# Kernel tuning notes

Hardware: AMD Instinct MI355X
Metric: run time of the kernel (lower is better)

The kernel has to match this reference:

```python
import jax, jax.numpy as jnp
import numpy as np

N_NODES = 100000


def _graph_conv(x, W, b, src, dst, norm):
    # DGL GraphConv(norm='left'): scale source features by 1/out_degree,
    # aggregate (sum over incoming edges). in_feats > out_feats so weight
    # multiply happens before aggregation (mathematically equivalent either way).
    h = x @ W  # [N, out]
    msg = (h * norm[:, None])[src]  # gather per-edge messages [E, out]
    agg = jax.ops.segment_sum(msg, dst, num_segments=N_NODES)
    return agg + b


def setup_inputs() -> dict:
    key = jax.random.key(0)
    ks = jax.random.split(key, 10)
    in_f, hid_f, out_f = 256, 128, 64
    n_edges = 1_600_000
    feat = jax.random.normal(ks[0], (N_NODES, in_f), dtype=jnp.float32)
    src = jax.random.randint(ks[1], (n_edges,), 0, N_NODES, dtype=jnp.int32)
    dst = jax.random.randint(ks[2], (n_edges,), 0, N_NODES, dtype=jnp.int32)
    noise = jax.random.normal(ks[3], (N_NODES, out_f), dtype=jnp.float32)
    s1 = 1.0 / np.sqrt(in_f)
    s2 = 1.0 / np.sqrt(hid_f)
    W_shared = jax.random.uniform(ks[4], (in_f, hid_f), minval=-s1, maxval=s1, dtype=jnp.float32)
    b_shared = jnp.zeros((hid_f,), jnp.float32)
    W_mu = jax.random.uniform(ks[5], (hid_f, out_f), minval=-s2, maxval=s2, dtype=jnp.float32)
    b_mu = jnp.zeros((out_f,), jnp.float32)
    W_ls = jax.random.uniform(ks[6], (hid_f, out_f), minval=-s2, maxval=s2, dtype=jnp.float32)
    b_ls = jnp.zeros((out_f,), jnp.float32)
    return {"feat": feat, "W_shared": W_shared, "b_shared": b_shared,
            "W_mu": W_mu, "b_mu": b_mu, "W_ls": W_ls, "b_ls": b_ls,
            "noise": noise, "src": src, "dst": dst}


def reference(feat, W_shared, b_shared, W_mu, b_mu, W_ls, b_ls, noise, src, dst):
    # left-norm: 1 / out_degree (clamped to >= 1, as DGL does)
    deg_out = jax.ops.segment_sum(jnp.ones_like(src, jnp.float32), src,
                                  num_segments=N_NODES)
    norm = 1.0 / jnp.maximum(deg_out, 1.0)
    # shared first GraphConv with ReLU activation
    h = jax.nn.relu(_graph_conv(feat, W_shared, b_shared, src, dst, norm))
    # two heads (no activation)
    mu = _graph_conv(h, W_mu, b_mu, src, dst, norm)
    log_sigma = _graph_conv(h, W_ls, b_ls, src, dst, norm)
    # reparameterized sample
    return mu + noise * jnp.exp(log_sigma)
```

## Files before the change

### kernel.cpp

```cpp
#include <hip/hip_runtime.h>
#include <hip/hip_bf16.h>
#include <math.h>

typedef __attribute__((ext_vector_type(8))) short short8;
typedef __attribute__((ext_vector_type(4))) float f32x4;

__device__ __forceinline__ unsigned short f2bf(float f) {
    unsigned int u = __float_as_uint(f);
    u += 0x7FFF + ((u >> 16) & 1);
    return (unsigned short)(u >> 16);
}
__device__ __forceinline__ float b2f(unsigned short s) {
    return __uint_as_float(((unsigned int)s) << 16);
}
__device__ __forceinline__ unsigned int f2bf2(float a, float b) {
    __hip_bfloat162 h = __float22bfloat162_rn(make_float2(a, b));
    return *(unsigned int*)&h;
}
__device__ __forceinline__ void gl_lds16(const void* g, void* l) {
    __builtin_amdgcn_global_load_lds(
        (const __attribute__((address_space(1))) void*)g,
        (__attribute__((address_space(3))) void*)l, 16, 0, 0);
}

#define EB 8192
#define BSH 10
#define NBKT 128

__global__ __launch_bounds__(256)
void k1_hist(const int* __restrict__ src, const int* __restrict__ dst,
             int* __restrict__ bhist, int* __restrict__ degS, int E) {
    __shared__ int hist[NBKT];
    int t = threadIdx.x;
    if (t < NBKT) hist[t] = 0;
    __syncthreads();
    int base = blockIdx.x * EB;
    int end = min(base + EB, E);
    for (int e = base + 4 * t; e < end; e += 1024) {
        if (e + 3 < end) {
            int4 d4 = *(const int4*)&dst[e];
            int4 s4 = *(const int4*)&src[e];
            atomicAdd(&hist[d4.x >> BSH], 1);
            atomicAdd(&hist[d4.y >> BSH], 1);
            atomicAdd(&hist[d4.z >> BSH], 1);
            atomicAdd(&hist[d4.w >> BSH], 1);
            atomicAdd(&degS[s4.x], 1);
            atomicAdd(&degS[s4.y], 1);
            atomicAdd(&degS[s4.z], 1);
            atomicAdd(&degS[s4.w], 1);
        } else {
            for (int q = e; q < end; ++q) {
                atomicAdd(&hist[dst[q] >> BSH], 1);
                atomicAdd(&degS[src[q]], 1);
            }
        }
    }
    __syncthreads();
    if (t < NBKT) bhist[(size_t)blockIdx.x * NBKT + t] = hist[t];
}

__global__ __launch_bounds__(128)
void kc1_totals(const int* __restrict__ bhist, int* __restrict__ totals, int PB) {
    int t = threadIdx.x;
    int slice = (PB + 7) / 8;
    int b0 = blockIdx.x * slice;
    int b1 = min(b0 + slice, PB);
    int s = 0;
    for (int blk = b0; blk < b1; ++blk) s += bhist[(size_t)blk * NBKT + t];
    if (s) atomicAdd(&totals[t], s);
}

__global__ __launch_bounds__(128)
void kc2_scan(const int* __restrict__ totals, int* __restrict__ bbase_d) {
    __shared__ int s[128];
    int t = threadIdx.x;
    int v = totals[t];
    s[t] = v;
    __syncthreads();
    for (int off = 1; off < 128; off <<= 1) {
        int u = (t >= off) ? s[t - off] : 0;
        __syncthreads();
        s[t] += u;
        __syncthreads();
    }
    bbase_d[t] = s[t] - v;
}

__global__ __launch_bounds__(256)
void kc3_boff(const int* __restrict__ bhist, const int* __restrict__ bbase_d,
              int* __restrict__ boffT, int PB) {
    __shared__ int sums[256];
    int b = blockIdx.x;
    int t = threadIdx.x;
    int v = (t < PB) ? bhist[(size_t)t * NBKT + b] : 0;
    sums[t] = v;
    __syncthreads();
    for (int off = 1; off < 256; off <<= 1) {
        int u = (t >= off) ? sums[t - off] : 0;
        __syncthreads();
        sums[t] += u;
        __syncthreads();
    }
    if (t < PB) boffT[(size_t)b * PB + t] = bbase_d[b] + sums[t] - v;
}

__global__ __launch_bounds__(256)
void k_norm(const int* __restrict__ degS, float* __restrict__ norm, int N) {
    int i = blockIdx.x * 256 + threadIdx.x;
    if (i < N) {
        int d = degS[i];
        norm[i] = 1.0f / (float)(d > 1 ? d : 1);
    }
}

__global__ __launch_bounds__(256)
void k2_scatter(const int* __restrict__ src, const int* __restrict__ dst,
                const int* __restrict__ boffT, int* __restrict__ parr,
                int E, int PB) {
    __shared__ int cnt[NBKT];
    int t = threadIdx.x;
    int blk = blockIdx.x;
    if (t < NBKT) cnt[t] = boffT[(size_t)t * PB + blk];
    __syncthreads();
    int base = blk * EB;
    int end = min(base + EB, E);
    for (int e = base + 4 * t; e < end; e += 1024) {
        if (e + 3 < end) {
            int4 s4 = *(const int4*)&src[e];
            int4 d4 = *(const int4*)&dst[e];
            int p0 = atomicAdd(&cnt[d4.x >> BSH], 1);
            parr[p0] = (s4.x << BSH) | (d4.x & (1024 - 1));
            int p1 = atomicAdd(&cnt[d4.y >> BSH], 1);
            parr[p1] = (s4.y << BSH) | (d4.y & (1024 - 1));
            int p2 = atomicAdd(&cnt[d4.z >> BSH], 1);
            parr[p2] = (s4.z << BSH) | (d4.z & (1024 - 1));
            int p3 = atomicAdd(&cnt[d4.w >> BSH], 1);
            parr[p3] = (s4.w << BSH) | (d4.w & (1024 - 1));
        } else {
            for (int q = e; q < end; ++q) {
                int sv = src[q], dv = dst[q];
                int pd = atomicAdd(&cnt[dv >> BSH], 1);
                parr[pd] = (sv << BSH) | (dv & (1024 - 1));
            }
        }
    }
}

__global__ __launch_bounds__(1024)
void k3_dst(const int* __restrict__ parr, const int* __restrict__ totals,
            const int* __restrict__ bbase_d, int* __restrict__ row_off,
            int* __restrict__ col, int N, int E) {
    __shared__ int hist[1024], sc[1024];
    int b = blockIdx.x, t = threadIdx.x;
    if (b == 0 && t == 0) row_off[N] = E;
    int ne = totals[b];
    int ebase = bbase_d[b];
    hist[t] = 0;
    __syncthreads();
    for (int i = t; i < ne; i += 1024)
        atomicAdd(&hist[parr[ebase + i] & 1023], 1);
    __syncthreads();
    int h = hist[t];
    sc[t] = h;
    __syncthreads();
    for (int off = 1; off < 1024; off <<= 1) {
        int u = (t >= off) ? sc[t - off] : 0;
        __syncthreads();
        sc[t] += u;
        __syncthreads();
    }
    int excl = sc[t] - h;
    int node = b * 1024 + t;
    if (node < N) row_off[node] = ebase + excl;
    hist[t] = ebase + excl;
    __syncthreads();
    for (int i = t; i < ne; i += 1024) {
        int pr = parr[ebase + i];
        int slot = atomicAdd(&hist[pr & 1023], 1);
        col[slot] = pr >> BSH;
    }
}


__global__ __launch_bounds__(256)
void k_wprep(const float* __restrict__ Wsh, const float* __restrict__ Wmu,
             const float* __restrict__ Wls, unsigned short* __restrict__ W1T,
             unsigned short* __restrict__ W2T) {
    int b = blockIdx.x, t = threadIdx.x;
    if (b < 128) {
        W1T[(size_t)b * 256 + t] = f2bf(Wsh[(size_t)t * 128 + b]);
    } else {
        int n = b - 128;
        if (t < 128) {
            float v = (n < 64) ? Wmu[(size_t)t * 64 + n]
                               : Wls[(size_t)t * 64 + (n - 64)];
            W2T[(size_t)n * 128 + t] = f2bf(v);
        }
    }
}

__global__ __launch_bounds__(256)
void k_gemm1(const float* __restrict__ A, int M,
             const unsigned short* __restrict__ W1T,
             const float* __restrict__ norm, unsigned short* __restrict__ outb) {
    __shared__ char ldsA[64 * 1040];
    const int w = threadIdx.x >> 6;
    const int lane = threadIdx.x & 63;
    const int quad = lane >> 4;
    const int l16 = lane & 15;
    const int cl = w * 16 + l16;
    const int r0 = blockIdx.x * 64;

#pragma unroll
    for (int i = 0; i < 16; ++i) {
        int row = r0 + w * 16 + i;
        if (row >= M) row = M - 1;
        const char* g = (const char*)A + (size_t)row * 1024 + lane * 16;
        char* l = ldsA + (w * 16 + i) * 1040 + lane * 16;
        gl_lds16(g, l);
    }

    short8 bw[2][8];
#pragma unroll
    for (int hf = 0; hf < 2; ++hf) {
        const unsigned short* wp = W1T + (size_t)(hf * 64 + cl) * 256 + quad * 8;
#pragma unroll
        for (int ks = 0; ks < 8; ++ks)
            bw[hf][ks] = *(const short8*)(wp + ks * 32);
    }
    __syncthreads();

    f32x4 acc[4][2];
#pragma unroll
    for (int m = 0; m < 4; ++m) {
        acc[m][0] = (f32x4){0.f, 0.f, 0.f, 0.f};
        acc[m][1] = (f32x4){0.f, 0.f, 0.f, 0.f};
    }
#pragma unroll
    for (int ks = 0; ks < 8; ++ks) {
#pragma unroll
        for (int m = 0; m < 4; ++m) {
            const float* pr = (const float*)(ldsA + (m * 16 + l16) * 1040 +
                                             (ks * 32 + quad * 8) * 4);
            float4 x = *(const float4*)pr;
            float4 y = *(const float4*)(pr + 4);
            union { short8 v; unsigned int u[4]; } c;
            c.u[0] = f2bf2(x.x, x.y);
            c.u[1] = f2bf2(x.z, x.w);
            c.u[2] = f2bf2(y.x, y.y);
            c.u[3] = f2bf2(y.z, y.w);
            acc[m][0] = __builtin_amdgcn_mfma_f32_16x16x32_bf16(bw[0][ks], c.v, acc[m][0], 0, 0, 0);
            acc[m][1] = __builtin_amdgcn_mfma_f32_16x16x32_bf16(bw[1][ks], c.v, acc[m][1], 0, 0, 0);
        }
    }
    const int colbase = w * 16 + quad * 4;
#pragma unroll
    for (int m = 0; m < 4; ++m) {
        int row = r0 + m * 16 + l16;
        if (row < M) {
            float nm = norm[row];
            ushort4 o0, o1;
            o0.x = f2bf(acc[m][0][0] * nm); o0.y = f2bf(acc[m][0][1] * nm);
            o0.z = f2bf(acc[m][0][2] * nm); o0.w = f2bf(acc[m][0][3] * nm);
            o1.x = f2bf(acc[m][1][0] * nm); o1.y = f2bf(acc[m][1][1] * nm);
            o1.z = f2bf(acc[m][1][2] * nm); o1.w = f2bf(acc[m][1][3] * nm);
            *(ushort4*)&outb[(size_t)row * 128 + colbase] = o0;
            *(ushort4*)&outb[(size_t)row * 128 + 64 + colbase] = o1;
        }
    }
}

__global__ __launch_bounds__(256)
void k_gemm2(const unsigned short* __restrict__ A, int M,
             const unsigned short* __restrict__ W2T,
             const float* __restrict__ norm, unsigned short* __restrict__ outb) {
    __shared__ char ldsB[16 * 1040];
    const int w = threadIdx.x >> 6;
    const int lane = threadIdx.x & 63;
    const int quad = lane >> 4;
    const int l16 = lane & 15;
    const int cl = w * 16 + l16;
    const int r0 = blockIdx.x * 64;

#pragma unroll
    for (int i = 0; i < 4; ++i) {
        int c = w * 4 + i;
        int crow = r0 + c * 4;
        if (crow + 4 > M) crow = M - 4;
        const char* g = (const char*)A + (size_t)crow * 256 + lane * 16;
        char* l = ldsB + c * 1040 + lane * 16;
        gl_lds16(g, l);
    }

    short8 bw[2][4];
#pragma unroll
    for (int hf = 0; hf < 2; ++hf) {
        const unsigned short* wp = W2T + (size_t)(hf * 64 + cl) * 128 + quad * 8;
#pragma unroll
        for (int ks = 0; ks < 4; ++ks)
            bw[hf][ks] = *(const short8*)(wp + ks * 32);
    }
    __syncthreads();

    f32x4 acc[4][2];
#pragma unroll
    for (int m = 0; m < 4; ++m) {
        acc[m][0] = (f32x4){0.f, 0.f, 0.f, 0.f};
        acc[m][1] = (f32x4){0.f, 0.f, 0.f, 0.f};
    }
#pragma unroll
    for (int ks = 0; ks < 4; ++ks) {
#pragma unroll
        for (int m = 0; m < 4; ++m) {
            int row = m * 16 + l16;
            short8 af = *(const short8*)(ldsB + (row >> 2) * 1040 + (row & 3) * 256 +
                                         (ks * 32 + quad * 8) * 2);
            acc[m][0] = __builtin_amdgcn_mfma_f32_16x16x32_bf16(bw[0][ks], af, acc[m][0], 0, 0, 0);
            acc[m][1] = __builtin_amdgcn_mfma_f32_16x16x32_bf16(bw[1][ks], af, acc[m][1], 0, 0, 0);
        }
    }
    const int colbase = w * 16 + quad * 4;
#pragma unroll
    for (int m = 0; m < 4; ++m) {
        int row = r0 + m * 16 + l16;
        if (row < M) {
            float nm = norm[row];
            ushort4 o0, o1;
            o0.x = f2bf(acc[m][0][0] * nm); o0.y = f2bf(acc[m][0][1] * nm);
            o0.z = f2bf(acc[m][0][2] * nm); o0.w = f2bf(acc[m][0][3] * nm);
            o1.x = f2bf(acc[m][1][0] * nm); o1.y = f2bf(acc[m][1][1] * nm);
            o1.z = f2bf(acc[m][1][2] * nm); o1.w = f2bf(acc[m][1][3] * nm);
            *(ushort4*)&outb[(size_t)row * 128 + colbase] = o0;
            *(ushort4*)&outb[(size_t)row * 128 + 64 + colbase] = o1;
        }
    }
}

__global__ __launch_bounds__(256)
void k_spmm_relu(const int* __restrict__ row_off, const int* __restrict__ col,
                 const unsigned short* __restrict__ hxb, const float* __restrict__ bias,
                 unsigned short* __restrict__ hb, int N) {
    int g = (blockIdx.x * blockDim.x + threadIdx.x) >> 5;
    int l = threadIdx.x & 31;
    if (g >= N) return;
    int e0 = row_off[g], e1 = row_off[g + 1];
    const ushort4* base = (const ushort4*)hxb;
    float4 acc = make_float4(0.f, 0.f, 0.f, 0.f);
    int e = e0;
    for (; e + 7 < e1; e += 8) {
        ushort4 v0 = base[(size_t)col[e] * 32 + l];
        ushort4 v1 = base[(size_t)col[e + 1] * 32 + l];
        ushort4 v2 = base[(size_t)col[e + 2] * 32 + l];
        ushort4 v3 = base[(size_t)col[e + 3] * 32 + l];
        ushort4 v4 = base[(size_t)col[e + 4] * 32 + l];
        ushort4 v5 = base[(size_t)col[e + 5] * 32 + l];
        ushort4 v6 = base[(size_t)col[e + 6] * 32 + l];
        ushort4 v7 = base[(size_t)col[e + 7] * 32 + l];
        acc.x += ((b2f(v0.x) + b2f(v1.x)) + (b2f(v2.x) + b2f(v3.x))) +
                 ((b2f(v4.x) + b2f(v5.x)) + (b2f(v6.x) + b2f(v7.x)));
        acc.y += ((b2f(v0.y) + b2f(v1.y)) + (b2f(v2.y) + b2f(v3.y))) +
                 ((b2f(v4.y) + b2f(v5.y)) + (b2f(v6.y) + b2f(v7.y)));
        acc.z += ((b2f(v0.z) + b2f(v1.z)) + (b2f(v2.z) + b2f(v3.z))) +
                 ((b2f(v4.z) + b2f(v5.z)) + (b2f(v6.z) + b2f(v7.z)));
        acc.w += ((b2f(v0.w) + b2f(v1.w)) + (b2f(v2.w) + b2f(v3.w))) +
                 ((b2f(v4.w) + b2f(v5.w)) + (b2f(v6.w) + b2f(v7.w)));
    }
    for (; e + 1 < e1; e += 2) {
        ushort4 a = base[(size_t)col[e] * 32 + l];
        ushort4 b = base[(size_t)col[e + 1] * 32 + l];
        acc.x += b2f(a.x) + b2f(b.x);
        acc.y += b2f(a.y) + b2f(b.y);
        acc.z += b2f(a.z) + b2f(b.z);
        acc.w += b2f(a.w) + b2f(b.w);
    }
    if (e < e1) {
        ushort4 a = base[(size_t)col[e] * 32 + l];
        acc.x += b2f(a.x); acc.y += b2f(a.y); acc.z += b2f(a.z); acc.w += b2f(a.w);
    }
    float4 bi = ((const float4*)bias)[l];
    ushort4 r;
    r.x = f2bf(fmaxf(acc.x + bi.x, 0.f));
    r.y = f2bf(fmaxf(acc.y + bi.y, 0.f));
    r.z = f2bf(fmaxf(acc.z + bi.z, 0.f));
    r.w = f2bf(fmaxf(acc.w + bi.w, 0.f));
    ((ushort4*)hb)[(size_t)g * 32 + l] = r;
}

__global__ __launch_bounds__(256)
void k_spmm_out(const int* __restrict__ row_off, const int* __restrict__ col,
                const unsigned short* __restrict__ hcb, const float* __restrict__ bmu,
                const float* __restrict__ bls, const float* __restrict__ noise,
                float* __restrict__ out, int N) {
    int g = (blockIdx.x * blockDim.x + threadIdx.x) >> 5;
    int l = threadIdx.x & 31;
    if (g >= N) return;
    int e0 = row_off[g], e1 = row_off[g + 1];
    const ushort4* base = (const ushort4*)hcb;
    float4 acc = make_float4(0.f, 0.f, 0.f, 0.f);
    int e = e0;
    for (; e + 7 < e1; e += 8) {
        ushort4 v0 = base[(size_t)col[e] * 32 + l];
        ushort4 v1 = base[(size_t)col[e + 1] * 32 + l];
        ushort4 v2 = base[(size_t)col[e + 2] * 32 + l];
        ushort4 v3 = base[(size_t)col[e + 3] * 32 + l];
        ushort4 v4 = base[(size_t)col[e + 4] * 32 + l];
        ushort4 v5 = base[(size_t)col[e + 5] * 32 + l];
        ushort4 v6 = base[(size_t)col[e + 6] * 32 + l];
        ushort4 v7 = base[(size_t)col[e + 7] * 32 + l];
        acc.x += ((b2f(v0.x) + b2f(v1.x)) + (b2f(v2.x) + b2f(v3.x))) +
                 ((b2f(v4.x) + b2f(v5.x)) + (b2f(v6.x) + b2f(v7.x)));
        acc.y += ((b2f(v0.y) + b2f(v1.y)) + (b2f(v2.y) + b2f(v3.y))) +
                 ((b2f(v4.y) + b2f(v5.y)) + (b2f(v6.y) + b2f(v7.y)));
        acc.z += ((b2f(v0.z) + b2f(v1.z)) + (b2f(v2.z) + b2f(v3.z))) +
                 ((b2f(v4.z) + b2f(v5.z)) + (b2f(v6.z) + b2f(v7.z)));
        acc.w += ((b2f(v0.w) + b2f(v1.w)) + (b2f(v2.w) + b2f(v3.w))) +
                 ((b2f(v4.w) + b2f(v5.w)) + (b2f(v6.w) + b2f(v7.w)));
    }
    for (; e + 1 < e1; e += 2) {
        ushort4 a = base[(size_t)col[e] * 32 + l];
        ushort4 b = base[(size_t)col[e + 1] * 32 + l];
        acc.x += b2f(a.x) + b2f(b.x);
        acc.y += b2f(a.y) + b2f(b.y);
        acc.z += b2f(a.z) + b2f(b.z);
        acc.w += b2f(a.w) + b2f(b.w);
    }
    if (e < e1) {
        ushort4 a = base[(size_t)col[e] * 32 + l];
        acc.x += b2f(a.x); acc.y += b2f(a.y); acc.z += b2f(a.z); acc.w += b2f(a.w);
    }
    int lane64 = threadIdx.x & 63;
    int p = (lane64 + 16) & 63;
    float lx = __shfl(acc.x, p, 64);
    float ly = __shfl(acc.y, p, 64);
    float lz = __shfl(acc.z, p, 64);
    float lw = __shfl(acc.w, p, 64);
    if (l < 16) {
        float4 bm = ((const float4*)bmu)[l];
        float4 bl = ((const float4*)bls)[l];
        float4 nz = ((const float4*)noise)[(size_t)g * 16 + l];
        float4 o;
        o.x = (acc.x + bm.x) + nz.x * expf(lx + bl.x);
        o.y = (acc.y + bm.y) + nz.y * expf(ly + bl.y);
        o.z = (acc.z + bm.z) + nz.z * expf(lz + bl.z);
        o.w = (acc.w + bm.w) + nz.w * expf(lw + bl.w);
        ((float4*)out)[(size_t)g * 16 + l] = o;
    }
}

static inline char* align64(char* p) {
    return (char*)(((uintptr_t)p + 63) & ~(uintptr_t)63);
}

extern "C" void kernel_launch(void* const* d_in, const int* in_sizes, int n_in,
                              void* d_out, int out_size, void* d_ws, size_t ws_size,
                              hipStream_t stream) {
    const float* feat  = (const float*)d_in[0];
    const float* Wsh   = (const float*)d_in[1];
    const float* bsh   = (const float*)d_in[2];
    const float* Wmu   = (const float*)d_in[3];
    const float* bmu   = (const float*)d_in[4];
    const float* Wls   = (const float*)d_in[5];
    const float* bls   = (const float*)d_in[6];
    const float* noise = (const float*)d_in[7];
    const int*   src   = (const int*)d_in[8];
    const int*   dst   = (const int*)d_in[9];
    float* out = (float*)d_out;

    const int N = in_sizes[0] / 256;
    const int E = in_sizes[8];
    const int PB = (E + EB - 1) / EB;

    char* p = (char*)d_ws;
    float* norm   = (float*)p;                  p += (size_t)N * 4;         p = align64(p);
    int* row_off  = (int*)p;                    p += (size_t)(N + 4) * 4;   p = align64(p);
    int* degS     = (int*)p;                    p += (size_t)N * 4;
    int* totals   = (int*)p;                    p += 128 * 4;
    int* bbase_d  = (int*)p;                    p += 128 * 4;               p = align64(p);
    unsigned short* W1T = (unsigned short*)p;   p += (size_t)128 * 256 * 2;
    unsigned short* W2T = (unsigned short*)p;   p += (size_t)128 * 128 * 2;
    p = align64(p);
    int* bhist    = (int*)p;                    p += (size_t)PB * NBKT * 4; p = align64(p);
    int* boffT    = (int*)p;                    p += (size_t)NBKT * PB * 4; p = align64(p);
    int* parr     = (int*)p;                    p += (size_t)E * 4;
    int* col      = (int*)p;                    p += (size_t)E * 4;         p = align64(p);
    unsigned short* hxb = (unsigned short*)p;
    unsigned short* hb  = (unsigned short*)d_out;

    hipMemsetAsync(degS, 0, (size_t)N * 4 + 128 * 4, stream);
    k_wprep<<<256, 256, 0, stream>>>(Wsh, Wmu, Wls, W1T, W2T);
    k1_hist<<<PB, 256, 0, stream>>>(src, dst, bhist, degS, E);
    kc1_totals<<<8, 128, 0, stream>>>(bhist, totals, PB);
    kc2_scan<<<1, 128, 0, stream>>>(totals, bbase_d);
    kc3_boff<<<NBKT, 256, 0, stream>>>(bhist, bbase_d, boffT, PB);
    k_norm<<<(N + 255) / 256, 256, 0, stream>>>(degS, norm, N);
    k2_scatter<<<PB, 256, 0, stream>>>(src, dst, boffT, parr, E, PB);
    k3_dst<<<NBKT, 1024, 0, stream>>>(parr, totals, bbase_d, row_off, col, N, E);

    int gtiles = (N + 63) / 64;
    k_gemm1<<<gtiles, 256, 0, stream>>>(feat, N, W1T, norm, hxb);
    k_spmm_relu<<<(N * 32 + 255) / 256, 256, 0, stream>>>(row_off, col, hxb, bsh, hb, N);
    k_gemm2<<<gtiles, 256, 0, stream>>>(hb, N, W2T, norm, hxb);
    k_spmm_out<<<(N * 32 + 255) / 256, 256, 0, stream>>>(row_off, col, hxb, bmu, bls, noise, out, N);
}
```

Baseline: 486.9 us.

## Compute out-degree via bucketed sort instead of global atomics; shrink buckets

Replaces the per-edge global atomicAdd on the out-degree array with a second bucketed counting pass over source ids: source bucket histograms sit next to the destination ones, edges are scattered into a 16-bit local-id array, and a new per-bucket kernel counts degrees in LDS and writes norm. It also shrinks buckets to 512 nodes and edge blocks to 2048 edges, which means more blocks and 1024-thread scans. The goal is to avoid contended random global atomics and the memset of the degree array, at the cost of extra scatter writes and an extra kernel launch.

Result: faster. 444.6 us (-8.7%).

```diff
diff --git a/kernel.cpp b/kernel.cpp
--- a/kernel.cpp
+++ b/kernel.cpp
@@ -23,16 +23,17 @@
         (__attribute__((address_space(3))) void*)l, 16, 0, 0);
 }
 
-#define EB 8192
-#define BSH 10
-#define NBKT 128
+#define EB 2048
+#define SH 9
+#define BSZ 512
 
 __global__ __launch_bounds__(256)
 void k1_hist(const int* __restrict__ src, const int* __restrict__ dst,
-             int* __restrict__ bhist, int* __restrict__ degS, int E) {
-    __shared__ int hist[NBKT];
+             int* __restrict__ bhist, int E, int NB2) {
+    __shared__ int hist[512];
     int t = threadIdx.x;
-    if (t < NBKT) hist[t] = 0;
+    int NB = NB2 >> 1;
+    for (int i = t; i < NB2; i += 256) hist[i] = 0;
     __syncthreads();
     int base = blockIdx.x * EB;
     int end = min(base + EB, E);
@@ -40,87 +41,84 @@
         if (e + 3 < end) {
             int4 d4 = *(const int4*)&dst[e];
             int4 s4 = *(const int4*)&src[e];
-            atomicAdd(&hist[d4.x >> BSH], 1);
-            atomicAdd(&hist[d4.y >> BSH], 1);
-            atomicAdd(&hist[d4.z >> BSH], 1);
-            atomicAdd(&hist[d4.w >> BSH], 1);
-            atomicAdd(&degS[s4.x], 1);
-            atomicAdd(&degS[s4.y], 1);
-            atomicAdd(&degS[s4.z], 1);
-            atomicAdd(&degS[s4.w], 1);
+            atomicAdd(&hist[d4.x >> SH], 1);
+            atomicAdd(&hist[d4.y >> SH], 1);
+            atomicAdd(&hist[d4.z >> SH], 1);
+            atomicAdd(&hist[d4.w >> SH], 1);
+            atomicAdd(&hist[NB + (s4.x >> SH)], 1);
+            atomicAdd(&hist[NB + (s4.y >> SH)], 1);
+            atomicAdd(&hist[NB + (s4.z >> SH)], 1);
+            atomicAdd(&hist[NB + (s4.w >> SH)], 1);
         } else {
             for (int q = e; q < end; ++q) {
-                atomicAdd(&hist[dst[q] >> BSH], 1);
-                atomicAdd(&degS[src[q]], 1);
+                atomicAdd(&hist[dst[q] >> SH], 1);
+                atomicAdd(&hist[NB + (src[q] >> SH)], 1);
             }
         }
     }
     __syncthreads();
-    if (t < NBKT) bhist[(size_t)blockIdx.x * NBKT + t] = hist[t];
-}
-
-__global__ __launch_bounds__(128)
-void kc1_totals(const int* __restrict__ bhist, int* __restrict__ totals, int PB) {
+    for (int i = t; i < NB2; i += 256)
+        bhist[(size_t)blockIdx.x * NB2 + i] = hist[i];
+}
+
+__global__ __launch_bounds__(512)
+void kc1_totals(const int* __restrict__ bhist, int* __restrict__ totals,
+                int PB, int NB2) {
     int t = threadIdx.x;
-    int slice = (PB + 7) / 8;
+    if (t >= NB2) return;
+    int slice = (PB + 15) / 16;
     int b0 = blockIdx.x * slice;
     int b1 = min(b0 + slice, PB);
     int s = 0;
-    for (int blk = b0; blk < b1; ++blk) s += bhist[(size_t)blk * NBKT + t];
+    for (int blk = b0; blk < b1; ++blk) s += bhist[(size_t)blk * NB2 + t];
     if (s) atomicAdd(&totals[t], s);
 }
 
-__global__ __launch_bounds__(128)
-void kc2_scan(const int* __restrict__ totals, int* __restrict__ bbase_d) {
-    __shared__ int s[128];
+__global__ __launch_bounds__(512)
+void kc2_scan(const int* __restrict__ totals, int* __restrict__ bbase, int NB) {
+    __shared__ int s[512];
     int t = threadIdx.x;
-    int v = totals[t];
+    int half = t >> 8;
+    int idx = t & 255;
+    int v = (idx < NB) ? totals[half * NB + idx] : 0;
     s[t] = v;
     __syncthreads();
-    for (int off = 1; off < 128; off <<= 1) {
-        int u = (t >= off) ? s[t - off] : 0;
+    for (int off = 1; off < 256; off <<= 1) {
+        int u = (idx >= off) ? s[t - off] : 0;
         __syncthreads();
         s[t] += u;
         __syncthreads();
     }
-    bbase_d[t] = s[t] - v;
-}
-
-__global__ __launch_bounds__(256)
-void kc3_boff(const int* __restrict__ bhist, const int* __restrict__ bbase_d,
-              int* __restrict__ boffT, int PB) {
-    __shared__ int sums[256];
+    if (idx < NB) bbase[half * NB + idx] = s[t] - v;
+}
+
+__global__ __launch_bounds__(1024)
+void kc3_boff(const int* __restrict__ bhist, const int* __restrict__ bbase,
+              int* __restrict__ boffT, int PB, int NB2) {
+    __shared__ int sums[1024];
     int b = blockIdx.x;
     int t = threadIdx.x;
-    int v = (t < PB) ? bhist[(size_t)t * NBKT + b] : 0;
+    int v = (t < PB) ? bhist[(size_t)t * NB2 + b] : 0;
     sums[t] = v;
     __syncthreads();
-    for (int off = 1; off < 256; off <<= 1) {
+    for (int off = 1; off < 1024; off <<= 1) {
         int u = (t >= off) ? sums[t - off] : 0;
         __syncthreads();
         sums[t] += u;
         __syncthreads();
     }
-    if (t < PB) boffT[(size_t)b * PB + t] = bbase_d[b] + sums[t] - v;
-}
-
-__global__ __launch_bounds__(256)
-void k_norm(const int* __restrict__ degS, float* __restrict__ norm, int N) {
-    int i = blockIdx.x * 256 + threadIdx.x;
-    if (i < N) {
-        int d = degS[i];
-        norm[i] = 1.0f / (float)(d > 1 ? d : 1);
-    }
+    if (t < PB) boffT[(size_t)b * PB + t] = bbase[b] + sums[t] - v;
 }
 
 __global__ __launch_bounds__(256)
 void k2_scatter(const int* __restrict__ src, const int* __restrict__ dst,
                 const int* __restrict__ boffT, int* __restrict__ parr,
-                int E, int PB) {
-    __shared__ int cnt[NBKT];
+                unsigned short* __restrict__ sarr, int E, int PB, int NB2) {
+    __shared__ int cnt[512];
     int t = threadIdx.x;
     int blk = blockIdx.x;
-    if (t < NBKT) cnt[t] = boffT[(size_t)t * PB + blk];
+    int NB = NB2 >> 1;
+    for (int i = t; i < NB2; i += 256) cnt[i] = boffT[(size_t)i * PB + blk];
     __syncthreads();
     int base = blk * EB;
     int end = min(base + EB, E);
@@ -128,19 +126,29 @@
         if (e + 3 < end) {
             int4 s4 = *(const int4*)&src[e];
             int4 d4 = *(const int4*)&dst[e];
-            int p0 = atomicAdd(&cnt[d4.x >> BSH], 1);
-            parr[p0] = (s4.x << BSH) | (d4.x & (1024 - 1));
-            int p1 = atomicAdd(&cnt[d4.y >> BSH], 1);
-            parr[p1] = (s4.y << BSH) | (d4.y & (1024 - 1));
-            int p2 = atomicAdd(&cnt[d4.z >> BSH], 1);
-            parr[p2] = (s4.z << BSH) | (d4.z & (1024 - 1));
-            int p3 = atomicAdd(&cnt[d4.w >> BSH], 1);
-            parr[p3] = (s4.w << BSH) | (d4.w & (1024 - 1));
+            int p0 = atomicAdd(&cnt[d4.x >> SH], 1);
+            parr[p0] = (s4.x << SH) | (d4.x & (BSZ - 1));
+            int p1 = atomicAdd(&cnt[d4.y >> SH], 1);
+            parr[p1] = (s4.y << SH) | (d4.y & (BSZ - 1));
+            int p2 = atomicAdd(&cnt[d4.z >> SH], 1);
+            parr[p2] = (s4.z << SH) | (d4.z & (BSZ - 1));
+            int p3 = atomicAdd(&cnt[d4.w >> SH], 1);
+            parr[p3] = (s4.w << SH) | (d4.w & (BSZ - 1));
+            int q0 = atomicAdd(&cnt[NB + (s4.x >> SH)], 1);
+            sarr[q0] = (unsigned short)(s4.x & (BSZ - 1));
+            int q1 = atomicAdd(&cnt[NB + (s4.y >> SH)], 1);
+            sarr[q1] = (unsigned short)(s4.y & (BSZ - 1));
+            int q2 = atomicAdd(&cnt[NB + (s4.z >> SH)], 1);
+            sarr[q2] = (unsigned short)(s4.z & (BSZ - 1));
+            int q3 = atomicAdd(&cnt[NB + (s4.w >> SH)], 1);
+            sarr[q3] = (unsigned short)(s4.w & (BSZ - 1));
         } else {
             for (int q = e; q < end; ++q) {
                 int sv = src[q], dv = dst[q];
-                int pd = atomicAdd(&cnt[dv >> BSH], 1);
-                parr[pd] = (sv << BSH) | (dv & (1024 - 1));
+                int pd = atomicAdd(&cnt[dv >> SH], 1);
+                parr[pd] = (sv << SH) | (dv & (BSZ - 1));
+                int ps = atomicAdd(&cnt[NB + (sv >> SH)], 1);
+                sarr[ps] = (unsigned short)(sv & (BSZ - 1));
             }
         }
     }
@@ -148,36 +156,57 @@
 
 __global__ __launch_bounds__(1024)
 void k3_dst(const int* __restrict__ parr, const int* __restrict__ totals,
-            const int* __restrict__ bbase_d, int* __restrict__ row_off,
+            const int* __restrict__ bbase, int* __restrict__ row_off,
             int* __restrict__ col, int N, int E) {
-    __shared__ int hist[1024], sc[1024];
+    __shared__ int hist[512], sc[512];
     int b = blockIdx.x, t = threadIdx.x;
     if (b == 0 && t == 0) row_off[N] = E;
     int ne = totals[b];
-    int ebase = bbase_d[b];
-    hist[t] = 0;
+    int ebase = bbase[b];
+    if (t < 512) hist[t] = 0;
     __syncthreads();
     for (int i = t; i < ne; i += 1024)
-        atomicAdd(&hist[parr[ebase + i] & 1023], 1);
-    __syncthreads();
-    int h = hist[t];
-    sc[t] = h;
-    __syncthreads();
-    for (int off = 1; off < 1024; off <<= 1) {
-        int u = (t >= off) ? sc[t - off] : 0;
+        atomicAdd(&hist[parr[ebase + i] & (BSZ - 1)], 1);
+    __syncthreads();
+    int h = 0;
+    if (t < 512) { h = hist[t]; sc[t] = h; }
+    __syncthreads();
+    for (int off = 1; off < 512; off <<= 1) {
+        int u = (t < 512 && t >= off) ? sc[t - off] : 0;
         __syncthreads();
-        sc[t] += u;
+        if (t < 512) sc[t] += u;
         __syncthreads();
     }
-    int excl = sc[t] - h;
-    int node = b * 1024 + t;
-    if (node < N) row_off[node] = ebase + excl;
-    hist[t] = ebase + excl;
+    if (t < 512) {
+        int excl = sc[t] - h;
+        int node = b * BSZ + t;
+        if (node < N) row_off[node] = ebase + excl;
+        hist[t] = ebase + excl;
+    }
     __syncthreads();
     for (int i = t; i < ne; i += 1024) {
         int pr = parr[ebase + i];
-        int slot = atomicAdd(&hist[pr & 1023], 1);
-        col[slot] = pr >> BSH;
+        int slot = atomicAdd(&hist[pr & (BSZ - 1)], 1);
+        col[slot] = pr >> SH;
+    }
+}
+
+__global__ __launch_bounds__(1024)
+void k3_src(const unsigned short* __restrict__ sarr, const int* __restrict__ totals_s,
+            const int* __restrict__ bbase_s, float* __restrict__ norm, int N) {
+    __shared__ int hist[512];
+    int b = blockIdx.x, t = threadIdx.x;
+    int ne = totals_s[b];
+    int sb = bbase_s[b];
+    if (t < 512) hist[t] = 0;
+    __syncthreads();
+    for (int i = t; i < ne; i += 1024)
+        atomicAdd(&hist[sarr[sb + i]], 1);
+    __syncthreads();
+    int node = b * BSZ + t;
+    if (t < 512 && node < N) {
+        int d = hist[t];
+        norm[node] = 1.0f / (float)(d > 1 ? d : 1);
     }
 }
 
@@ -469,32 +498,34 @@
     const int N = in_sizes[0] / 256;
     const int E = in_sizes[8];
     const int PB = (E + EB - 1) / EB;
+    const int NB = (N + BSZ - 1) / BSZ;
+    const int NB2 = 2 * NB;
 
     char* p = (char*)d_ws;
-    float* norm   = (float*)p;                  p += (size_t)N * 4;         p = align64(p);
-    int* row_off  = (int*)p;                    p += (size_t)(N + 4) * 4;   p = align64(p);
-    int* degS     = (int*)p;                    p += (size_t)N * 4;
-    int* totals   = (int*)p;                    p += 128 * 4;
-    int* bbase_d  = (int*)p;                    p += 128 * 4;               p = align64(p);
+    float* norm   = (float*)p;                  p += (size_t)N * 4;          p = align64(p);
+    int* row_off  = (int*)p;                    p += (size_t)(N + 4) * 4;    p = align64(p);
+    int* totals   = (int*)p;                    p += 512 * 4;
+    int* bbase    = (int*)p;                    p += 512 * 4;                p = align64(p);
     unsigned short* W1T = (unsigned short*)p;   p += (size_t)128 * 256 * 2;
     unsigned short* W2T = (unsigned short*)p;   p += (size_t)128 * 128 * 2;
     p = align64(p);
-    int* bhist    = (int*)p;                    p += (size_t)PB * NBKT * 4; p = align64(p);
-    int* boffT    = (int*)p;                    p += (size_t)NBKT * PB * 4; p = align64(p);
+    int* bhist    = (int*)p;                    p += (size_t)PB * NB2 * 4;   p = align64(p);
+    int* boffT    = (int*)p;                    p += (size_t)NB2 * PB * 4;   p = align64(p);
     int* parr     = (int*)p;                    p += (size_t)E * 4;
-    int* col      = (int*)p;                    p += (size_t)E * 4;         p = align64(p);
+    unsigned short* sarr = (unsigned short*)p;  p += (size_t)E * 2;          p = align64(p);
+    int* col      = (int*)p;                    p += (size_t)E * 4;          p = align64(p);
     unsigned short* hxb = (unsigned short*)p;
     unsigned short* hb  = (unsigned short*)d_out;
 
-    hipMemsetAsync(degS, 0, (size_t)N * 4 + 128 * 4, stream);
+    hipMemsetAsync(totals, 0, 512 * sizeof(int), stream);
     k_wprep<<<256, 256, 0, stream>>>(Wsh, Wmu, Wls, W1T, W2T);
-    k1_hist<<<PB, 256, 0, stream>>>(src, dst, bhist, degS, E);
-    kc1_totals<<<8, 128, 0, stream>>>(bhist, totals, PB);
-    kc2_scan<<<1, 128, 0, stream>>>(totals, bbase_d);
-    kc3_boff<<<NBKT, 256, 0, stream>>>(bhist, bbase_d, boffT, PB);
-    k_norm<<<(N + 255) / 256, 256, 0, stream>>>(degS, norm, N);
-    k2_scatter<<<PB, 256, 0, stream>>>(src, dst, boffT, parr, E, PB);
-    k3_dst<<<NBKT, 1024, 0, stream>>>(parr, totals, bbase_d, row_off, col, N, E);
+    k1_hist<<<PB, 256, 0, stream>>>(src, dst, bhist, E, NB2);
+    kc1_totals<<<16, 512, 0, stream>>>(bhist, totals, PB, NB2);
+    kc2_scan<<<1, 512, 0, stream>>>(totals, bbase, NB);
+    kc3_boff<<<NB2, 1024, 0, stream>>>(bhist, bbase, boffT, PB, NB2);
+    k2_scatter<<<PB, 256, 0, stream>>>(src, dst, boffT, parr, sarr, E, PB, NB2);
+    k3_dst<<<NB, 1024, 0, stream>>>(parr, totals, bbase, row_off, col, N, E);
+    k3_src<<<NB, 1024, 0, stream>>>(sarr, totals + NB, bbase + NB, norm, N);
 
     int gtiles = (N + 63) / 64;
     k_gemm1<<<gtiles, 256, 0, stream>>>(feat, N, W1T, norm, hxb);
```
